# Kernel tuning notes

Measured on AMD Instinct MI355X. Metric: run time of the kernel, lower is better.

Reference implementation:

```python
import jax, jax.numpy as jnp
import numpy as np

B, CTX, QST, E, H = 8, 4096, 512, 300, 128

def setup_inputs() -> dict:
    key = jax.random.key(0)
    k1, k2, k3, k4 = jax.random.split(key, 4)
    context_sequence = jax.random.normal(k1, (B, CTX, E), dtype=jnp.float32)
    question_sequence = jax.random.normal(k2, (B, QST, E), dtype=jnp.float32)
    question_mask = jnp.ones((B, QST), dtype=jnp.int32)
    # dense layer params (PyTorch Linear: y = x @ W.T + b)
    bound = 1.0 / np.sqrt(E)
    W = jax.random.uniform(k3, (H, E), minval=-bound, maxval=bound, dtype=jnp.float32)
    b = jax.random.uniform(k4, (H,), minval=-bound, maxval=bound, dtype=jnp.float32)
    return {"context_sequence": context_sequence, "question_sequence": question_sequence,
            "question_mask": question_mask, "W": W, "b": b}

def reference(context_sequence, question_sequence, question_mask, W, b):
    # ReLU(dense(x)) for both sequences
    ctx_logits = jax.nn.relu(jnp.einsum('bce,he->bch', context_sequence, W) + b)   # [B, CTX, H]
    qst_logits = jax.nn.relu(jnp.einsum('bqe,he->bqh', question_sequence, W) + b)  # [B, QST, H]
    scores = jnp.einsum('bch,bqh->bcq', ctx_logits, qst_logits)                    # [B, CTX, QST]
    scores = jnp.where(question_mask[:, None, :] == 0, -jnp.inf, scores)
    attn = jax.nn.softmax(scores, axis=-1)
    return jnp.einsum('bcq,bqh->bch', attn, qst_logits)                            # [B, CTX, H]
```

## Files before the change

### kernel.cpp

```cpp
#include <hip/hip_runtime.h>
#include <hip/hip_bf16.h>

#define BB   8
#define SCTX 4096
#define SQ   512
#define EE   300
#define HH   128
#define EP   320
#define CST  328
#define LOG2E 1.4426950408889634f

typedef short bhalf4 __attribute__((ext_vector_type(4)));
typedef short short8 __attribute__((ext_vector_type(8)));
typedef float f32x4  __attribute__((ext_vector_type(4)));
typedef unsigned u32x4 __attribute__((ext_vector_type(4)));

#define MFMA16(a, b, c) __builtin_amdgcn_mfma_f32_16x16x32_bf16((a), (b), (c), 0, 0, 0)
#define SBAR()   __builtin_amdgcn_s_barrier()
#define SCHED0() __builtin_amdgcn_sched_barrier(0)

__device__ __forceinline__ short f2bf(float f) {
  unsigned u = __builtin_bit_cast(unsigned, f);
  u += 0x7fffu + ((u >> 16) & 1u);
  return (short)(u >> 16);
}
__device__ __forceinline__ float bf2f(short s) {
  return __builtin_bit_cast(float, ((unsigned)(unsigned short)s) << 16);
}
__device__ __forceinline__ unsigned pack2(float a, float b) {
  return (unsigned)(unsigned short)f2bf(a) | ((unsigned)(unsigned short)f2bf(b) << 16);
}
__device__ __forceinline__ void gload16(const void* g, void* lds) {
  __builtin_amdgcn_global_load_lds(
      (const __attribute__((address_space(1))) void*)g,
      (__attribute__((address_space(3))) void*)lds, 16, 0, 0);
}

__global__ void k_wpad(const float* __restrict__ W, short* __restrict__ wsw) {
  const int h = blockIdx.x, k = threadIdx.x;
  float v = (k < EE) ? W[h * EE + k] : 0.0f;
  const int m = h >> 4, t = h & 15, kk = k >> 5, quad = (k >> 3) & 3, j = k & 7;
  wsw[((kk * 8 + m) * 64 + quad * 16 + t) * 8 + j] = f2bf(v);
}

__global__ __launch_bounds__(256) void k_qlog(const float* __restrict__ qst,
                                              const short* __restrict__ wsw,
                                              const float* __restrict__ bias,
                                              short* __restrict__ ql,
                                              short* __restrict__ qlT) {
  const int b = blockIdx.y;
  const int m0 = blockIdx.x * 32;
  const int tid = threadIdx.x;
  const int w = tid >> 6, l = tid & 63, t = l & 15, quad = l >> 4;
  const int g = w >> 1, hf = w & 1;

  __shared__ __align__(16) short cst[32 * CST];

  const float4* cbase = (const float4*)(qst + (size_t)(b * SQ + m0) * EE);
#pragma unroll
  for (int j = 0; j < 10; ++j) {
    int i4 = tid + j * 256;
    if (i4 < 2400) {
      float4 v = cbase[i4];
      int row = i4 / 75, c4 = i4 - row * 75;
      bhalf4 s4; s4[0] = f2bf(v.x); s4[1] = f2bf(v.y); s4[2] = f2bf(v.z); s4[3] = f2bf(v.w);
      *(bhalf4*)(cst + row * CST + c4 * 4) = s4;
    }
  }
  for (int i = tid; i < 320; i += 256) {
    int row = i / 10, c = (i - row * 10) * 2;
    *(int*)&cst[row * CST + 300 + c] = 0;
  }
  __syncthreads();

  const short* arow = cst + (g * 16 + t) * CST;
  f32x4 acc[4] = {};
#pragma unroll
  for (int kk = 0; kk < 10; ++kk) {
    const int k = kk * 32 + quad * 8;
    short8 a = *(const short8*)(arow + k);
    short8 w8[4];
#pragma unroll
    for (int n = 0; n < 4; ++n)
      w8[n] = *(const short8*)(wsw + ((kk * 8 + hf * 4 + n) * 64 + l) * 8);
#pragma unroll
    for (int n = 0; n < 4; ++n) acc[n] = MFMA16(a, w8[n], acc[n]);
  }
#pragma unroll
  for (int n = 0; n < 4; ++n) {
    const int h = (hf * 4 + n) * 16 + t;
    const float bv = bias[h];
    bhalf4 s4;
#pragma unroll
    for (int r = 0; r < 4; ++r) {
      float v = fmaxf(acc[n][r] + bv, 0.0f);
      short s16 = f2bf(v);
      s4[r] = s16;
      const int row = m0 + g * 16 + quad * 4 + r;
      ql[((size_t)b * SQ + row) * HH + h] = s16;
    }
    *(bhalf4*)&qlT[((size_t)b * HH + h) * SQ + m0 + g * 16 + quad * 4] = s4;
  }
}

__global__ __launch_bounds__(256, 2) void k_attn(const float* __restrict__ ctx,
                                                 const short* __restrict__ wsw,
                                                 const float* __restrict__ bias,
                                                 const int* __restrict__ mask,
                                                 const short* __restrict__ ql,
                                                 const short* __restrict__ qlT,
                                                 float* __restrict__ out) {
  const int b = blockIdx.y;
  const int m0 = blockIdx.x * 64;
  const int tid = threadIdx.x;
  const int w = tid >> 6, l = tid & 63, t = l & 15, quad = l >> 4;
  const int g = w >> 1, hf = w & 1;

  __shared__ __align__(16) short uq[16384];
  __shared__ __align__(16) short uv[16384];
  __shared__ __align__(16) short maskh[SQ];
  short* cst = uq;
  short* clt = uv;
  short* qb0 = uq;          short* qb1 = uq + 8192;
  short* vb0 = uv;          short* vb1 = uv + 8192;

  for (int i = tid; i < SQ; i += 256)
    maskh[i] = f2bf(mask[b * SQ + i] ? -8.0f : -1e30f);

  for (int i = 0; i < 2; ++i) {
    const float4* cbase = (const float4*)(ctx + ((size_t)b * SCTX + m0 + i * 32) * EE);
#pragma unroll
    for (int j = 0; j < 10; ++j) {
      int i4 = tid + j * 256;
      if (i4 < 2400) {
        float4 v = cbase[i4];
        int row = i4 / 75, c4 = i4 - row * 75;
        bhalf4 s4; s4[0] = f2bf(v.x); s4[1] = f2bf(v.y); s4[2] = f2bf(v.z); s4[3] = f2bf(v.w);
        *(bhalf4*)(cst + row * CST + c4 * 4) = s4;
      }
    }
    for (int k = tid; k < 320; k += 256) {
      int row = k / 10, c = (k - row * 10) * 2;
      *(int*)&cst[row * CST + 300 + c] = 0;
    }
    __syncthreads();
    const short* arow = cst + (g * 16 + t) * CST;
    f32x4 acc[4] = {};
#pragma unroll
    for (int kk = 0; kk < 10; ++kk) {
      const int k = kk * 32 + quad * 8;
      short8 a = *(const short8*)(arow + k);
      short8 w8[4];
#pragma unroll
      for (int n = 0; n < 4; ++n)
        w8[n] = *(const short8*)(wsw + ((kk * 8 + hf * 4 + n) * 64 + l) * 8);
#pragma unroll
      for (int n = 0; n < 4; ++n) acc[n] = MFMA16(a, w8[n], acc[n]);
    }
#pragma unroll
    for (int n = 0; n < 4; ++n) {
      const int h = (hf * 4 + n) * 16 + t;
      const float bv = bias[h];
#pragma unroll
      for (int r = 0; r < 4; ++r) {
        float v = fmaxf(acc[n][r] + bv, 0.0f);
        clt[(i * 32 + g * 16 + quad * 4 + r) * 136 + h] = f2bf(v);
      }
    }
    __syncthreads();
  }

  short8 af[4];
#pragma unroll
  for (int kk = 0; kk < 4; ++kk)
    af[kk] = *(const short8*)&clt[(w * 16 + t) * 136 + kk * 32 + quad * 8];
  __syncthreads();

  const int srcA = ((quad & 1) * 2) * 16 + t;
  const int srcB = srcA + 16;
  const bool hiq = quad >= 2;
  const int sx  = (t & 7) << 3;
  const int rl4 = l >> 4;
  const int cbq = (l & 15) * 16;
  const int rl8 = l >> 3;
  const int cbv = (l & 7) * 16;

  auto stageTo = [&](short* qb, short* vb, int c) {
#pragma unroll
    for (int s = 0; s < 4; ++s) {
      const int row = w * 16 + s * 4 + rl4;
      gload16((const char*)(ql + ((size_t)b * SQ + c * 64 + row) * HH) +
                  (cbq ^ ((row & 7) << 4)),
              qb + (w * 16 + s * 4) * 128);
    }
#pragma unroll
    for (int s = 0; s < 4; ++s) {
      const int row = w * 32 + s * 8 + rl8;
      gload16((const char*)(qlT + ((size_t)b * HH + row) * SQ + c * 64) +
                  (cbv ^ ((row & 7) << 4)),
              vb + (w * 32 + s * 8) * 64);
    }
  };

  stageTo(qb0, vb0, 0);
  stageTo(qb1, vb1, 1);

  f32x4 o[8] = {};
  float rtot = 0.0f;
  for (int c = 0; c < 8; ++c) {
    short* qch = (c & 1) ? qb1 : qb0;
    short* vch = (c & 1) ? vb1 : vb0;
    if (c < 7) { asm volatile("s_waitcnt vmcnt(8)" ::: "memory"); }
    else       { asm volatile("s_waitcnt vmcnt(0)" ::: "memory"); }
    SCHED0(); SBAR(); SCHED0();

    f32x4 sv[4] = {};
#pragma unroll
    for (int n2 = 0; n2 < 4; ++n2) {
      const short* qr = qch + (n2 * 16 + t) * 128;
#pragma unroll
      for (int kx = 0; kx < 4; ++kx) {
        short8 b8 = *(const short8*)(qr + ((kx * 32 + quad * 8) ^ sx));
        sv[n2] = MFMA16(b8, af[kx], sv[n2]);
      }
    }
    unsigned pk[8];
#pragma unroll
    for (int n2 = 0; n2 < 4; ++n2) {
      bhalf4 mb = *(const bhalf4*)&maskh[c * 64 + n2 * 16 + quad * 4];
      float p0 = exp2f((sv[n2][0] + bf2f(mb[0])) * LOG2E);
      float p1 = exp2f((sv[n2][1] + bf2f(mb[1])) * LOG2E);
      float p2 = exp2f((sv[n2][2] + bf2f(mb[2])) * LOG2E);
      float p3 = exp2f((sv[n2][3] + bf2f(mb[3])) * LOG2E);
      rtot += (p0 + p1) + (p2 + p3);
      pk[n2 * 2 + 0] = pack2(p0, p1);
      pk[n2 * 2 + 1] = pack2(p2, p3);
    }
    unsigned sA[8], sB[8];
#pragma unroll
    for (int i = 0; i < 8; ++i) {
      sA[i] = (unsigned)__shfl((int)pk[i], srcA);
      sB[i] = (unsigned)__shfl((int)pk[i], srcB);
    }
#pragma unroll
    for (int kk2 = 0; kk2 < 2; ++kk2) {
      u32x4 av;
      av[0] = hiq ? sA[kk2 * 4 + 2] : sA[kk2 * 4 + 0];
      av[1] = hiq ? sA[kk2 * 4 + 3] : sA[kk2 * 4 + 1];
      av[2] = hiq ? sB[kk2 * 4 + 2] : sB[kk2 * 4 + 0];
      av[3] = hiq ? sB[kk2 * 4 + 3] : sB[kk2 * 4 + 1];
      short8 pa = __builtin_bit_cast(short8, av);
      const int co = (kk2 * 32 + quad * 8) ^ sx;
#pragma unroll
      for (int n = 0; n < 8; ++n) {
        short8 v8 = *(const short8*)&vch[(n * 16 + t) * 64 + co];
        o[n] = MFMA16(pa, v8, o[n]);
      }
    }
    if (c < 7) {
      asm volatile("s_waitcnt lgkmcnt(0)" ::: "memory");
      SCHED0(); SBAR(); SCHED0();
      if (c < 6) stageTo(qch, vch, c + 2);
    }
  }

  rtot += __shfl_xor(rtot, 16);
  rtot += __shfl_xor(rtot, 32);
  f32x4 rinv;
#pragma unroll
  for (int r = 0; r < 4; ++r) rinv[r] = 1.0f / __shfl(rtot, quad * 4 + r);
  float* obase = out + ((size_t)b * SCTX + m0 + w * 16) * HH;
#pragma unroll
  for (int n = 0; n < 8; ++n)
#pragma unroll
    for (int r = 0; r < 4; ++r)
      obase[(quad * 4 + r) * HH + n * 16 + t] = o[n][r] * rinv[r];
}

extern "C" void kernel_launch(void* const* d_in, const int* in_sizes, int n_in,
                              void* d_out, int out_size, void* d_ws, size_t ws_size,
                              hipStream_t stream) {
  const float* ctx  = (const float*)d_in[0];
  const float* qst  = (const float*)d_in[1];
  const int*   mask = (const int*)d_in[2];
  const float* W    = (const float*)d_in[3];
  const float* bias = (const float*)d_in[4];
  float* out = (float*)d_out;

  short* wsw  = (short*)d_ws;
  short* ql   = (short*)((char*)d_ws + 81920);
  short* qlT  = ql + (size_t)BB * SQ * HH;

  k_wpad<<<dim3(HH), dim3(EP), 0, stream>>>(W, wsw);
  k_qlog<<<dim3(SQ / 32, BB), dim3(256), 0, stream>>>(qst, wsw, bias, ql, qlT);
  k_attn<<<dim3(SCTX / 64, BB), dim3(256), 0, stream>>>(ctx, wsw, bias, mask, ql, qlT, out);
}
```

Before: 121.2 us.

## Fuse weight swizzle into question-logit kernel and drop one launch

```diff
diff --git a/kernel.cpp b/kernel.cpp
--- a/kernel.cpp
+++ b/kernel.cpp
@@ -6,7 +6,6 @@
 #define SQ   512
 #define EE   300
 #define HH   128
-#define EP   320
 #define CST  328
 #define LOG2E 1.4426950408889634f
 
@@ -36,70 +35,88 @@
       (__attribute__((address_space(3))) void*)lds, 16, 0, 0);
 }
 
-__global__ void k_wpad(const float* __restrict__ W, short* __restrict__ wsw) {
-  const int h = blockIdx.x, k = threadIdx.x;
-  float v = (k < EE) ? W[h * EE + k] : 0.0f;
-  const int m = h >> 4, t = h & 15, kk = k >> 5, quad = (k >> 3) & 3, j = k & 7;
-  wsw[((kk * 8 + m) * 64 + quad * 16 + t) * 8 + j] = f2bf(v);
-}
-
 __global__ __launch_bounds__(256) void k_qlog(const float* __restrict__ qst,
-                                              const short* __restrict__ wsw,
+                                              const float* __restrict__ W,
                                               const float* __restrict__ bias,
                                               short* __restrict__ ql,
-                                              short* __restrict__ qlT) {
+                                              short* __restrict__ qlT,
+                                              short* __restrict__ wsw) {
   const int b = blockIdx.y;
-  const int m0 = blockIdx.x * 32;
+  const int q0 = blockIdx.x * 16;
   const int tid = threadIdx.x;
   const int w = tid >> 6, l = tid & 63, t = l & 15, quad = l >> 4;
-  const int g = w >> 1, hf = w & 1;
-
-  __shared__ __align__(16) short cst[32 * CST];
-
-  const float4* cbase = (const float4*)(qst + (size_t)(b * SQ + m0) * EE);
-#pragma unroll
-  for (int j = 0; j < 10; ++j) {
+
+  __shared__ __align__(16) short cst[16 * CST];
+
+  const float4* cbase = (const float4*)(qst + (size_t)(b * SQ + q0) * EE);
+#pragma unroll
+  for (int j = 0; j < 5; ++j) {
     int i4 = tid + j * 256;
-    if (i4 < 2400) {
+    if (i4 < 1200) {
       float4 v = cbase[i4];
       int row = i4 / 75, c4 = i4 - row * 75;
       bhalf4 s4; s4[0] = f2bf(v.x); s4[1] = f2bf(v.y); s4[2] = f2bf(v.z); s4[3] = f2bf(v.w);
       *(bhalf4*)(cst + row * CST + c4 * 4) = s4;
     }
   }
-  for (int i = tid; i < 320; i += 256) {
+  for (int i = tid; i < 160; i += 256) {
     int row = i / 10, c = (i - row * 10) * 2;
     *(int*)&cst[row * CST + 300 + c] = 0;
   }
+  if (b == 0) {
+    const int h = blockIdx.x * 4;
+#pragma unroll
+    for (int j = 0; j < 5; ++j) {
+      int i = tid + j * 256;
+      int hi = i / 320, k = i - hi * 320;
+      float v = (k < EE) ? W[(h + hi) * EE + k] : 0.0f;
+      int m = (h + hi) >> 4, tt = (h + hi) & 15, kk = k >> 5, qq = (k >> 3) & 3, jj = k & 7;
+      wsw[((kk * 8 + m) * 64 + qq * 16 + tt) * 8 + jj] = f2bf(v);
+    }
+  }
   __syncthreads();
 
-  const short* arow = cst + (g * 16 + t) * CST;
-  f32x4 acc[4] = {};
+  f32x4 acc1[2] = {}, acc2[2] = {};
+  const short* arow = cst + t * CST;
 #pragma unroll
   for (int kk = 0; kk < 10; ++kk) {
-    const int k = kk * 32 + quad * 8;
-    short8 a = *(const short8*)(arow + k);
-    short8 w8[4];
-#pragma unroll
-    for (int n = 0; n < 4; ++n)
-      w8[n] = *(const short8*)(wsw + ((kk * 8 + hf * 4 + n) * 64 + l) * 8);
-#pragma unroll
-    for (int n = 0; n < 4; ++n) acc[n] = MFMA16(a, w8[n], acc[n]);
-  }
-#pragma unroll
-  for (int n = 0; n < 4; ++n) {
-    const int h = (hf * 4 + n) * 16 + t;
-    const float bv = bias[h];
-    bhalf4 s4;
-#pragma unroll
-    for (int r = 0; r < 4; ++r) {
-      float v = fmaxf(acc[n][r] + bv, 0.0f);
-      short s16 = f2bf(v);
-      s4[r] = s16;
-      const int row = m0 + g * 16 + quad * 4 + r;
-      ql[((size_t)b * SQ + row) * HH + h] = s16;
-    }
-    *(bhalf4*)&qlT[((size_t)b * HH + h) * SQ + m0 + g * 16 + quad * 4] = s4;
+    short8 a = *(const short8*)(arow + kk * 32 + quad * 8);
+#pragma unroll
+    for (int n = 0; n < 2; ++n) {
+      const int habs = (w * 2 + n) * 16;
+      short8 w8;
+      if (kk < 9) {
+        const float* wrow = W + (size_t)(habs + t) * EE + kk * 32 + quad * 8;
+        float4 f0 = *(const float4*)(wrow);
+        float4 f1 = *(const float4*)(wrow + 4);
+        w8[0] = f2bf(f0.x); w8[1] = f2bf(f0.y); w8[2] = f2bf(f0.z); w8[3] = f2bf(f0.w);
+        w8[4] = f2bf(f1.x); w8[5] = f2bf(f1.y); w8[6] = f2bf(f1.z); w8[7] = f2bf(f1.w);
+      } else {
+#pragma unroll
+        for (int jj = 0; jj < 8; ++jj) {
+          int k = 288 + quad * 8 + jj;
+          w8[jj] = (k < EE) ? f2bf(W[(size_t)(habs + t) * EE + k]) : (short)0;
+        }
+      }
+      acc1[n] = MFMA16(a, w8, acc1[n]);
+      acc2[n] = MFMA16(w8, a, acc2[n]);
+    }
+  }
+#pragma unroll
+  for (int n = 0; n < 2; ++n) {
+    const int habs = (w * 2 + n) * 16;
+    const float bv1 = bias[habs + t];
+    bhalf4 s1;
+#pragma unroll
+    for (int r = 0; r < 4; ++r) s1[r] = f2bf(fmaxf(acc1[n][r] + bv1, 0.0f));
+    *(bhalf4*)&qlT[((size_t)b * HH + habs + t) * SQ + q0 + quad * 4] = s1;
+    const float4 bv2 = *(const float4*)(bias + habs + quad * 4);
+    bhalf4 s2;
+    s2[0] = f2bf(fmaxf(acc2[n][0] + bv2.x, 0.0f));
+    s2[1] = f2bf(fmaxf(acc2[n][1] + bv2.y, 0.0f));
+    s2[2] = f2bf(fmaxf(acc2[n][2] + bv2.z, 0.0f));
+    s2[3] = f2bf(fmaxf(acc2[n][3] + bv2.w, 0.0f));
+    *(bhalf4*)&ql[((size_t)b * SQ + q0 + t) * HH + habs + quad * 4] = s2;
   }
 }
 
@@ -291,7 +308,6 @@
   short* ql   = (short*)((char*)d_ws + 81920);
   short* qlT  = ql + (size_t)BB * SQ * HH;
 
-  k_wpad<<<dim3(HH), dim3(EP), 0, stream>>>(W, wsw);
-  k_qlog<<<dim3(SQ / 32, BB), dim3(256), 0, stream>>>(qst, wsw, bias, ql, qlT);
+  k_qlog<<<dim3(SQ / 16, BB), dim3(256), 0, stream>>>(qst, W, bias, ql, qlT, wsw);
   k_attn<<<dim3(SCTX / 64, BB), dim3(256), 0, stream>>>(ctx, wsw, bias, mask, ql, qlT, out);
 }
```

Result: slower. 124.5 us (+2.8%).
